# Kernel tuning notes

Measured on AMD Instinct MI355X. Metric: run time of the kernel, lower is better.

The kernel has to match this reference:

```python
import jax, jax.numpy as jnp
import numpy as np

V, E, H2, T = 50000, 256, 512, 16  # vocab, embed, hidden_dim, tagset
H = H2 // 2                        # per-direction hidden
START, STOP = 14, 15
NEG = -10000.0


def setup_inputs() -> dict:
    key = jax.random.key(0)
    ks = jax.random.split(key, 13)
    s = 0.08
    tokens = jax.random.randint(ks[0], (32, 512), 0, V)
    embed_table = jax.random.normal(ks[1], (V, E), jnp.float32)
    Wi_f = jax.random.normal(ks[2], (4 * H, E), jnp.float32) * s
    Wh_f = jax.random.normal(ks[3], (4 * H, H), jnp.float32) * s
    bi_f = jnp.zeros((4 * H,), jnp.float32)
    bh_f = jnp.zeros((4 * H,), jnp.float32)
    Wi_b = jax.random.normal(ks[4], (4 * H, E), jnp.float32) * s
    Wh_b = jax.random.normal(ks[5], (4 * H, H), jnp.float32) * s
    bi_b = jnp.zeros((4 * H,), jnp.float32)
    bh_b = jnp.zeros((4 * H,), jnp.float32)
    Wt = jax.random.normal(ks[6], (T, H2), jnp.float32) * s
    bt = jnp.zeros((T,), jnp.float32)
    trans = jax.random.normal(ks[7], (T, T), jnp.float32)
    trans = trans.at[START, :].set(NEG).at[:, STOP].set(NEG)
    return {"tokens": tokens, "embed_table": embed_table,
            "Wi_f": Wi_f, "Wh_f": Wh_f, "bi_f": bi_f, "bh_f": bh_f,
            "Wi_b": Wi_b, "Wh_b": Wh_b, "bi_b": bi_b, "bh_b": bh_b,
            "Wt": Wt, "bt": bt, "transitions": trans}


def _lstm_dir(x, Wi, Wh, bi, bh, reverse=False):
    # x: [S, B, E] -> h seq [S, B, H], PyTorch gate order i,f,g,o
    S, B, _ = x.shape
    xs = x[::-1] if reverse else x
    pre = jnp.einsum('sbe,ge->sbg', xs, Wi) + bi + bh  # precompute input GEMM

    def step(carry, z_t):
        h, c = carry
        z = z_t + h @ Wh.T  # [B, 4H]
        i, f, g, o = jnp.split(z, 4, axis=-1)
        c = jax.nn.sigmoid(f) * c + jax.nn.sigmoid(i) * jnp.tanh(g)
        h = jax.nn.sigmoid(o) * jnp.tanh(c)
        return (h, c), h

    h0 = jnp.zeros((B, H), x.dtype)
    _, hs = jax.lax.scan(step, (h0, h0), pre)
    return hs[::-1] if reverse else hs


def reference(tokens, embed_table, Wi_f, Wh_f, bi_f, bh_f,
              Wi_b, Wh_b, bi_b, bh_b, Wt, bt, transitions):
    x = embed_table[tokens]                # [B, S, E]
    x = jnp.transpose(x, (1, 0, 2))        # [S, B, E] seq-first like nn.LSTM
    hf = _lstm_dir(x, Wi_f, Wh_f, bi_f, bh_f, reverse=False)
    hb = _lstm_dir(x, Wi_b, Wh_b, bi_b, bh_b, reverse=True)
    feats = jnp.concatenate([hf, hb], axis=-1)           # [S, B, 2H]
    emissions = jnp.einsum('sbh,th->sbt', feats, Wt) + bt  # [S, B, T]

    B = tokens.shape[0]
    alpha0 = jnp.full((B, T), NEG, jnp.float32).at[:, START].set(0.0)

    def crf_step(alpha, emit_t):
        # alpha: [B, T_prev]; transitions[next, prev]; emit_t: [B, T_next]
        scores = alpha[:, None, :] + transitions[None, :, :] + emit_t[:, :, None]
        return jax.nn.logsumexp(scores, axis=2), None

    alpha, _ = jax.lax.scan(crf_step, alpha0, emissions)
    log_Z = jax.nn.logsumexp(alpha + transitions[STOP][None, :], axis=1)  # [B]
    return log_Z
```

## Files before the change

kernel.cpp:

```cpp
#include <hip/hip_runtime.h>
#include <hip/hip_bf16.h>
#include <stdint.h>

typedef __attribute__((ext_vector_type(4))) float f32x4;
typedef __attribute__((ext_vector_type(8))) short bf16x8;

#define SENT 0xFFFFFFFFFFFFFFFFULL

#define WS_XBF   0u
#define WS_WIR   8388608u
#define WS_BIAS  9437184u
#define WS_PRE   9445376u
#define WS_HALL  76554240u
#define WS_EMIS  93368320u
#define WS_CHK   94416896u

__device__ __forceinline__ unsigned short f2bf(float x) {
    union { float f; unsigned int u; } v; v.f = x;
    return (unsigned short)((v.u + 0x7FFFu + ((v.u >> 16) & 1u)) >> 16);
}
__device__ __forceinline__ float bf2f(unsigned short b) {
    union { float f; unsigned int u; } v; v.u = ((unsigned int)b) << 16; return v.f;
}
__device__ __forceinline__ unsigned int pack2(float a, float b) {
    return (unsigned int)f2bf(a) | ((unsigned int)f2bf(b) << 16);
}
__device__ __forceinline__ float sigf(float x)  { return 1.0f / (1.0f + __expf(-x)); }
__device__ __forceinline__ float tanhf_(float x){ return 1.0f - 2.0f / (__expf(2.0f * x) + 1.0f); }

__global__ __launch_bounds__(256) void k_prep(
    const int* __restrict__ tokens, const float* __restrict__ embed,
    const float* __restrict__ Wi_f, const float* __restrict__ Wi_b,
    const float* __restrict__ bi_f, const float* __restrict__ bh_f,
    const float* __restrict__ bi_b, const float* __restrict__ bh_b,
    char* __restrict__ ws)
{
    int blk = blockIdx.x, tid = threadIdx.x;
    unsigned short* xbf  = (unsigned short*)(ws + WS_XBF);
    unsigned short* wir  = (unsigned short*)(ws + WS_WIR);
    float* biasr         = (float*)(ws + WS_BIAS);
    if (blk < 2048) {
        int rr = tid >> 5, cc = tid & 31;
        int r = blk * 8 + rr;
        int s = r >> 5, b = r & 31;
        int tok = tokens[b * 512 + s];
        int k = cc * 8;
        const float* src = embed + (size_t)tok * 256 + k;
        float4 a = *(const float4*)src;
        float4 c = *(const float4*)(src + 4);
        uint4 o; o.x = pack2(a.x, a.y); o.y = pack2(a.z, a.w);
        o.z = pack2(c.x, c.y); o.w = pack2(c.z, c.w);
        *(uint4*)(xbf + (size_t)r * 256 + k) = o;
    } else if (blk < 2304) {
        int rr = tid >> 5, cc = tid & 31;
        int rowp = (blk - 2048) * 8 + rr;
        int dir = rowp >> 10, q = rowp & 1023;
        int j = q >> 8, rs = q & 255;
        int g = rs >> 6, hl = rs & 63;
        int srow = g * 256 + j * 64 + hl;
        const float* W = dir ? Wi_b : Wi_f;
        int k = cc * 8;
        const float* src = W + (size_t)srow * 256 + k;
        float4 a = *(const float4*)src;
        float4 c = *(const float4*)(src + 4);
        uint4 o; o.x = pack2(a.x, a.y); o.y = pack2(a.z, a.w);
        o.z = pack2(c.x, c.y); o.w = pack2(c.z, c.w);
        *(uint4*)(wir + (size_t)rowp * 256 + k) = o;
        if (cc == 0)
            biasr[rowp] = dir ? (bi_b[srow] + bh_b[srow]) : (bi_f[srow] + bh_f[srow]);
    } else {
        size_t g = (size_t)(blk - 2304) * 256 + tid;
        uint4* hall4 = (uint4*)(ws + WS_HALL);
        const unsigned int NF = 0xFFFFFFFFu;
        for (size_t u = g; u < 1050624u; u += 65536u) {
            size_t slot = (u >> 10) % 513u;
            uint4 val;
            if (slot == 0) { val.x = 0u; val.y = 0u; val.z = 0u; val.w = 0u; }
            else           { val.x = NF; val.y = NF; val.z = NF; val.w = NF; }
            hall4[u] = val;
        }
    }
}

__global__ __launch_bounds__(256) void k_pregemm(char* __restrict__ ws)
{
    __shared__ unsigned short Asb[128 * 136];
    __shared__ unsigned short Bsb[64 * 136];
    const unsigned short* xbf = (const unsigned short*)(ws + WS_XBF);
    const unsigned short* wir = (const unsigned short*)(ws + WS_WIR);
    const float* biasr        = (const float*)(ws + WS_BIAS);
    unsigned short* pre       = (unsigned short*)(ws + WS_PRE);
    int blk = blockIdx.x, tid = threadIdx.x;
    int mb = blk >> 5, nb = blk & 31;
    int Mbase = mb * 128, Nbase = nb * 64;
    int w = tid >> 6, l = tid & 63, col = l & 15, quad = l >> 4;
    f32x4 acc[4][2];
    #pragma unroll
    for (int a = 0; a < 4; ++a)
        #pragma unroll
        for (int b = 0; b < 2; ++b) acc[a][b] = (f32x4){0.f, 0.f, 0.f, 0.f};

    for (int kh = 0; kh < 2; ++kh) {
        __syncthreads();
        #pragma unroll
        for (int i = 0; i < 8; ++i) {
            int c = tid + i * 256;
            int row = c >> 4, c16 = c & 15;
            uint4 v = *(const uint4*)(xbf + ((size_t)(Mbase + row) * 256 + kh * 128 + c16 * 8));
            *(uint4*)(Asb + row * 136 + c16 * 8) = v;
        }
        #pragma unroll
        for (int i = 0; i < 4; ++i) {
            int c = tid + i * 256;
            int row = c >> 4, c16 = c & 15;
            uint4 v = *(const uint4*)(wir + ((size_t)(Nbase + row) * 256 + kh * 128 + c16 * 8));
            *(uint4*)(Bsb + row * 136 + c16 * 8) = v;
        }
        __syncthreads();
        int mhalf = w >> 1, nh = w & 1;
        #pragma unroll
        for (int kt = 0; kt < 4; ++kt) {
            bf16x8 bfr[2];
            #pragma unroll
            for (int nn = 0; nn < 2; ++nn)
                bfr[nn] = *(const bf16x8*)(Bsb + (16 * (nh * 2 + nn) + col) * 136 + kt * 32 + quad * 8);
            #pragma unroll
            for (int mm = 0; mm < 4; ++mm) {
                bf16x8 afr = *(const bf16x8*)(Asb + (16 * (mhalf * 4 + mm) + col) * 136 + kt * 32 + quad * 8);
                #pragma unroll
                for (int nn = 0; nn < 2; ++nn)
                    acc[mm][nn] = __builtin_amdgcn_mfma_f32_16x16x32_bf16(afr, bfr[nn], acc[mm][nn], 0, 0, 0);
            }
        }
    }
    #pragma unroll
    for (int mm = 0; mm < 4; ++mm) {
        int m_t = (w >> 1) * 4 + mm;
        int s = (Mbase >> 5) + (m_t >> 1);
        int bhalf = m_t & 1;
        #pragma unroll
        for (int nn = 0; nn < 2; ++nn) {
            int ncol = Nbase + 16 * ((w & 1) * 2 + nn) + col;
            int dir = ncol >> 10, j = (ncol >> 8) & 3, r = ncol & 255;
            int g = r >> 6, hl16 = (r >> 4) & 3;
            int tidp = (bhalf * 4 + hl16) * 64 + l;
            float bv = biasr[ncol];
            f32x4 a = acc[mm][nn];
            uint2 o;
            o.x = pack2(a[0] + bv, a[1] + bv);
            o.y = pack2(a[2] + bv, a[3] + bv);
            size_t off = (((size_t)(dir * 512 + s) * 4 + j) * 512 + tidp) * 16 + g * 4;
            *(uint2*)(pre + off) = o;
        }
    }
}

__global__ __launch_bounds__(512, 2) void k_rec(
    const float* __restrict__ Wh_f, const float* __restrict__ Wh_b, char* __restrict__ ws)
{
    __shared__ unsigned short hbuf[32 * 264];
    __shared__ unsigned short hst[8 * 16 * 20];
    int blk = blockIdx.x, tid = threadIdx.x;
    int dir = blk >> 2, j = blk & 3;
    int w = tid >> 6, l = tid & 63, col = l & 15, quad = l >> 4;
    int m = w >> 2, hl16 = w & 3;
    const float* Wh = dir ? Wh_b : Wh_f;
    const unsigned short* pre = (const unsigned short*)(ws + WS_PRE);
    unsigned short* hall      = (unsigned short*)(ws + WS_HALL);

    bf16x8 wf[4][8];
    #pragma unroll
    for (int g = 0; g < 4; ++g) {
        int grow = g * 256 + j * 64 + hl16 * 16 + col;
        #pragma unroll
        for (int kt = 0; kt < 8; ++kt) {
            const float* src = Wh + (size_t)grow * 256 + kt * 32 + quad * 8;
            float4 x0 = *(const float4*)src;
            float4 x1 = *(const float4*)(src + 4);
            bf16x8 f;
            f[0] = (short)f2bf(x0.x); f[1] = (short)f2bf(x0.y);
            f[2] = (short)f2bf(x0.z); f[3] = (short)f2bf(x0.w);
            f[4] = (short)f2bf(x1.x); f[5] = (short)f2bf(x1.y);
            f[6] = (short)f2bf(x1.z); f[7] = (short)f2bf(x1.w);
            wf[g][kt] = f;
        }
    }
    for (int u = tid; u < 1280; u += 512) ((unsigned int*)hst)[u] = 0;
    __syncthreads();

    float cst[4] = {0.f, 0.f, 0.f, 0.f};
    size_t hbase_u = (size_t)dir * 513 * 8192;

    for (int st = 0; st < 512; ++st) {
        int s = dir ? (511 - st) : st;
        const uint4* pp = (const uint4*)(pre + ((((size_t)(dir * 512 + s)) * 4 + j) * 512 + tid) * 16);
        uint4 p0 = pp[0], p1 = pp[1];

        unsigned short* hsl = hall + hbase_u + (size_t)st * 8192;
        unsigned long long v[4];
        int rows[4], c8s[4];
        bool own[4];
        #pragma unroll
        for (int i = 0; i < 4; ++i) {
            int q = tid + i * 512;
            int row = q >> 6, c8 = q & 63;
            rows[i] = row; c8s[i] = c8;
            own[i] = (c8 >= j * 16) && (c8 < j * 16 + 16);
            if (!own[i])
                v[i] = __hip_atomic_fetch_add((unsigned long long*)(hsl + (size_t)q * 4), 0ULL,
                                              __ATOMIC_RELAXED, __HIP_MEMORY_SCOPE_AGENT);
        }
        #pragma unroll
        for (int i = 0; i < 4; ++i) {
            if (own[i]) {
                int lc = c8s[i] * 4 - j * 64;
                int hl = lc >> 4, c4 = lc & 15;
                int wp = (rows[i] >> 4) * 4 + hl, r_in = rows[i] & 15;
                v[i] = *(const unsigned long long*)(hst + wp * 320 + r_in * 20 + c4);
            } else {
                while (v[i] == SENT)
                    v[i] = __hip_atomic_fetch_add((unsigned long long*)(hsl + (size_t)(tid + i * 512) * 4),
                                                  0ULL, __ATOMIC_RELAXED, __HIP_MEMORY_SCOPE_AGENT);
            }
        }
        #pragma unroll
        for (int i = 0; i < 4; ++i)
            *(unsigned long long*)(hbuf + rows[i] * 264 + c8s[i] * 4) = v[i];
        __syncthreads();

        f32x4 acc[4];
        #pragma unroll
        for (int g = 0; g < 4; ++g) acc[g] = (f32x4){0.f, 0.f, 0.f, 0.f};
        #pragma unroll
        for (int kt = 0; kt < 8; ++kt) {
            bf16x8 af = *(const bf16x8*)(hbuf + (m * 16 + col) * 264 + kt * 32 + quad * 8);
            #pragma unroll
            for (int g = 0; g < 4; ++g)
                acc[g] = __builtin_amdgcn_mfma_f32_16x16x32_bf16(af, wf[g][kt], acc[g], 0, 0, 0);
        }
        unsigned int pw[8] = {p0.x, p0.y, p0.z, p0.w, p1.x, p1.y, p1.z, p1.w};
        float z[4][4];
        #pragma unroll
        for (int g = 0; g < 4; ++g) {
            #pragma unroll
            for (int r2 = 0; r2 < 2; ++r2) {
                unsigned int u = pw[g * 2 + r2];
                z[g][r2 * 2]     = acc[g][r2 * 2]     + bf2f((unsigned short)(u & 0xffff));
                z[g][r2 * 2 + 1] = acc[g][r2 * 2 + 1] + bf2f((unsigned short)(u >> 16));
            }
        }
        unsigned short hb16[4];
        #pragma unroll
        for (int r = 0; r < 4; ++r) {
            float ci = sigf(z[1][r]) * cst[r] + sigf(z[0][r]) * tanhf_(z[2][r]);
            cst[r] = ci;
            hb16[r] = f2bf(sigf(z[3][r]) * tanhf_(ci));
        }
        unsigned short* hw = hst + w * 320;
        #pragma unroll
        for (int r = 0; r < 4; ++r) hw[(quad * 4 + r) * 20 + col] = hb16[r];
        int rrow = l >> 2, cpart = l & 3;
        unsigned long long hv = *(const unsigned long long*)(hw + rrow * 20 + cpart * 4);
        size_t dsto = hbase_u + (size_t)(st + 1) * 8192 + (size_t)(m * 16 + rrow) * 256
                    + j * 64 + hl16 * 16 + cpart * 4;
        (void)__hip_atomic_exchange((unsigned long long*)(hall + dsto), hv,
                                    __ATOMIC_RELAXED, __HIP_MEMORY_SCOPE_AGENT);
        __syncthreads();
    }
}

__global__ __launch_bounds__(256) void k_emis(
    const float* __restrict__ Wt, const float* __restrict__ bt, char* __restrict__ ws)
{
    __shared__ float WtL[16 * 528];
    __shared__ unsigned short hrow[16 * 536];
    __shared__ float btL[16];
    int blk = blockIdx.x, tid = threadIdx.x;
    int sbb = blk * 16;
    int s = sbb >> 5, bbase = sbb & 31;
    const unsigned short* hall = (const unsigned short*)(ws + WS_HALL);
    float* emis = (float*)(ws + WS_EMIS);
    #pragma unroll
    for (int i = 0; i < 8; ++i) {
        int c = tid + i * 256;
        int trow = c >> 7, c128 = c & 127;
        float4 v = *(const float4*)(Wt + (size_t)trow * 512 + c128 * 4);
        *(float4*)(WtL + trow * 528 + c128 * 4) = v;
    }
    #pragma unroll
    for (int i = 0; i < 4; ++i) {
        int c = tid + i * 256;
        int row = c >> 6, c6 = c & 63, half = c6 >> 5, c16 = c6 & 31;
        size_t base = half == 0 ? (size_t)(s + 1) * 8192 : ((size_t)513 + (512 - s)) * 8192;
        uint4 v = *(const uint4*)(hall + base + (size_t)(bbase + row) * 256 + c16 * 8);
        *(uint4*)(hrow + row * 536 + half * 256 + c16 * 8) = v;
    }
    if (tid < 16) btL[tid] = bt[tid];
    __syncthreads();
    int t = tid >> 4, i = tid & 15;
    float acc = btL[t];
    const float* wrow = WtL + t * 528;
    const unsigned short* hr = hrow + i * 536;
    #pragma unroll 8
    for (int k = 0; k < 512; k += 4) {
        uint2 hu = *(const uint2*)(hr + k);
        float4 wv = *(const float4*)(wrow + k);
        acc += bf2f((unsigned short)(hu.x & 0xffff)) * wv.x
             + bf2f((unsigned short)(hu.x >> 16))    * wv.y
             + bf2f((unsigned short)(hu.y & 0xffff)) * wv.z
             + bf2f((unsigned short)(hu.y >> 16))    * wv.w;
    }
    emis[((size_t)(bbase + i) * 512 + s) * 16 + t] = acc;
}

__global__ __launch_bounds__(256) void k_crfc(const float* __restrict__ trans, char* __restrict__ ws)
{
    __shared__ float trL[16 * 17];
    __shared__ float est[16 * 16];
    __shared__ float Pb[2][16 * 17];
    int blk = blockIdx.x, tid = threadIdx.x;
    int b = blk >> 5, c = blk & 31;
    int t = tid >> 4, p = tid & 15;
    const float* emis = (const float*)(ws + WS_EMIS);
    float* chk = (float*)(ws + WS_CHK);
    trL[t * 17 + p] = trans[t * 16 + p];
    est[t * 16 + p] = emis[((size_t)b * 512 + c * 16 + t) * 16 + p];
    __syncthreads();
    float tr[16];
    #pragma unroll
    for (int q = 0; q < 16; ++q) tr[q] = trL[t * 17 + q];
    float out = trL[t * 17 + p] + est[0 * 16 + t];
    Pb[0][t * 17 + p] = out;
    __syncthreads();
    int cur = 0;
    for (int si = 1; si < 16; ++si) {
        float v[16]; float mx = -3.0e38f;
        #pragma unroll
        for (int q = 0; q < 16; ++q) { v[q] = tr[q] + Pb[cur][q * 17 + p]; mx = fmaxf(mx, v[q]); }
        float ss = 0.f;
        #pragma unroll
        for (int q = 0; q < 16; ++q) ss += __expf(v[q] - mx);
        out = est[si * 16 + t] + mx + __logf(ss);
        Pb[1 - cur][t * 17 + p] = out;
        __syncthreads();
        cur = 1 - cur;
    }
    chk[(size_t)(b * 32 + c) * 256 + t * 16 + p] = out;
}

__global__ __launch_bounds__(256) void k_crff(
    const float* __restrict__ trans, char* __restrict__ ws, float* __restrict__ out)
{
    __shared__ float Cst[16 * 17];
    __shared__ float Pb[2][16 * 17];
    __shared__ float af[16];
    int b = blockIdx.x, tid = threadIdx.x;
    int t = tid >> 4, p = tid & 15;
    const float* chk = (const float*)(ws + WS_CHK);
    Pb[0][t * 17 + p] = chk[(size_t)(b * 32) * 256 + t * 16 + p];
    __syncthreads();
    int cur = 0;
    for (int ci = 1; ci < 32; ++ci) {
        Cst[t * 17 + p] = chk[(size_t)(b * 32 + ci) * 256 + t * 16 + p];
        __syncthreads();
        float v[16]; float mx = -3.0e38f;
        #pragma unroll
        for (int q = 0; q < 16; ++q) { v[q] = Cst[t * 17 + q] + Pb[cur][q * 17 + p]; mx = fmaxf(mx, v[q]); }
        float ss = 0.f;
        #pragma unroll
        for (int q = 0; q < 16; ++q) ss += __expf(v[q] - mx);
        float outv = mx + __logf(ss);
        Pb[1 - cur][t * 17 + p] = outv;
        __syncthreads();
        cur = 1 - cur;
    }
    float vfin = Pb[cur][t * 17 + p] + ((p == 14) ? 0.0f : -10000.0f);
    Cst[t * 17 + p] = vfin;
    __syncthreads();
    if (tid < 16) {
        float mx = -3.0e38f;
        for (int q = 0; q < 16; ++q) mx = fmaxf(mx, Cst[tid * 17 + q]);
        float ss = 0.f;
        for (int q = 0; q < 16; ++q) ss += __expf(Cst[tid * 17 + q] - mx);
        af[tid] = mx + __logf(ss) + trans[15 * 16 + tid];
    }
    __syncthreads();
    if (tid == 0) {
        float mx = -3.0e38f;
        for (int q = 0; q < 16; ++q) mx = fmaxf(mx, af[q]);
        float ss = 0.f;
        for (int q = 0; q < 16; ++q) ss += __expf(af[q] - mx);
        out[b] = mx + __logf(ss);
    }
}

extern "C" void kernel_launch(void* const* d_in, const int* in_sizes, int n_in,
                              void* d_out, int out_size, void* d_ws, size_t ws_size,
                              hipStream_t stream)
{
    const int*   tokens = (const int*)d_in[0];
    const float* embed  = (const float*)d_in[1];
    const float* Wi_f   = (const float*)d_in[2];
    const float* Wh_f   = (const float*)d_in[3];
    const float* bi_f   = (const float*)d_in[4];
    const float* bh_f   = (const float*)d_in[5];
    const float* Wi_b   = (const float*)d_in[6];
    const float* Wh_b   = (const float*)d_in[7];
    const float* bi_b   = (const float*)d_in[8];
    const float* bh_b   = (const float*)d_in[9];
    const float* Wt     = (const float*)d_in[10];
    const float* bt     = (const float*)d_in[11];
    const float* trans  = (const float*)d_in[12];
    char* ws = (char*)d_ws;
    float* out = (float*)d_out;

    hipLaunchKernelGGL(k_prep, dim3(2560), dim3(256), 0, stream,
                       tokens, embed, Wi_f, Wi_b, bi_f, bh_f, bi_b, bh_b, ws);
    hipLaunchKernelGGL(k_pregemm, dim3(4096), dim3(256), 0, stream, ws);
    hipLaunchKernelGGL(k_rec, dim3(8), dim3(512), 0, stream, Wh_f, Wh_b, ws);
    hipLaunchKernelGGL(k_emis, dim3(1024), dim3(256), 0, stream, Wt, bt, ws);
    hipLaunchKernelGGL(k_crfc, dim3(1024), dim3(256), 0, stream, trans, ws);
    hipLaunchKernelGGL(k_crff, dim3(32), dim3(256), 0, stream, trans, ws, out);
}
```

Measured before the change: 1.608 ms.

## Co-locate recurrence blocks on one XCD and use workgroup-scope polling

The recurrent kernel now launches 128 blocks. Each block reads its XCC_ID and claims a slot through atomic counters, and the first XCD to gather 8 blocks takes all 8 recurrence roles while the remaining blocks exit. Because all cooperating blocks then share one XCD's L2, the cross-block hidden-state exchange switches to workgroup-scope atomics (CAS-based polling and exchange), which avoids the slower device-scope coherence traffic on every timestep. The polling loop is also restructured per thread with bounded retries. This relies on an assumption about XCD cache sharing and on enough blocks landing on one XCD; if no XCD gathers 8 blocks in time, or scope semantics differ from the assumption, the result could be wrong or the kernel could stall.

```diff
diff --git a/kernel.cpp b/kernel.cpp
--- a/kernel.cpp
+++ b/kernel.cpp
@@ -12,6 +12,7 @@
 #define WS_BIAS  9437184u
 #define WS_PRE   9445376u
 #define WS_HALL  76554240u
+#define WS_CTL   93364224u
 #define WS_EMIS  93368320u
 #define WS_CHK   94416896u
 
@@ -69,6 +70,8 @@
         if (cc == 0)
             biasr[rowp] = dir ? (bi_b[srow] + bh_b[srow]) : (bi_f[srow] + bh_f[srow]);
     } else {
+        if (blk == 2304 && tid < 16)
+            ((unsigned int*)(ws + WS_CTL))[tid] = 0u;
         size_t g = (size_t)(blk - 2304) * 256 + tid;
         uint4* hall4 = (uint4*)(ws + WS_HALL);
         const unsigned int NF = 0xFFFFFFFFu;
@@ -160,8 +163,37 @@
 {
     __shared__ unsigned short hbuf[32 * 264];
     __shared__ unsigned short hst[8 * 16 * 20];
-    int blk = blockIdx.x, tid = threadIdx.x;
-    int dir = blk >> 2, j = blk & 3;
+    __shared__ int sRole;
+    int tid = threadIdx.x;
+
+    if (tid == 0) {
+        int xcd;
+        asm volatile("s_getreg_b32 %0, hwreg(HW_REG_XCC_ID)" : "=s"(xcd));
+        xcd &= 7;
+        unsigned int* ctl = (unsigned int*)(ws + WS_CTL);
+        unsigned int slot = __hip_atomic_fetch_add(&ctl[xcd], 1u,
+                              __ATOMIC_RELAXED, __HIP_MEMORY_SCOPE_AGENT);
+        int role = -1;
+        if (slot < 8u) {
+            if (slot == 7u) {
+                unsigned int expv = 0u;
+                __hip_atomic_compare_exchange_strong(&ctl[8], &expv, (unsigned int)(xcd + 1),
+                    __ATOMIC_RELAXED, __ATOMIC_RELAXED, __HIP_MEMORY_SCOPE_AGENT);
+            }
+            unsigned int ts; long gc = 0;
+            do {
+                ts = __hip_atomic_fetch_add(&ctl[8], 0u,
+                        __ATOMIC_RELAXED, __HIP_MEMORY_SCOPE_AGENT);
+            } while (ts == 0u && ++gc < (1L << 26));
+            if (ts == (unsigned int)(xcd + 1)) role = (int)slot;
+        }
+        sRole = role;
+    }
+    __syncthreads();
+    int role = sRole;
+    if (role < 0) return;
+    int dir = role >> 2, j = role & 3;
+
     int w = tid >> 6, l = tid & 63, col = l & 15, quad = l >> 4;
     int m = w >> 2, hl16 = w & 3;
     const float* Wh = dir ? Wh_b : Wh_f;
@@ -190,6 +222,8 @@
 
     float cst[4] = {0.f, 0.f, 0.f, 0.f};
     size_t hbase_u = (size_t)dir * 513 * 8192;
+    int row0 = tid >> 6, c8 = tid & 63;
+    bool ownl = (c8 >= j * 16) && (c8 < j * 16 + 16);
 
     for (int st = 0; st < 512; ++st) {
         int s = dir ? (511 - st) : st;
@@ -198,34 +232,44 @@
 
         unsigned short* hsl = hall + hbase_u + (size_t)st * 8192;
         unsigned long long v[4];
-        int rows[4], c8s[4];
-        bool own[4];
-        #pragma unroll
-        for (int i = 0; i < 4; ++i) {
-            int q = tid + i * 512;
-            int row = q >> 6, c8 = q & 63;
-            rows[i] = row; c8s[i] = c8;
-            own[i] = (c8 >= j * 16) && (c8 < j * 16 + 16);
-            if (!own[i])
-                v[i] = __hip_atomic_fetch_add((unsigned long long*)(hsl + (size_t)q * 4), 0ULL,
-                                              __ATOMIC_RELAXED, __HIP_MEMORY_SCOPE_AGENT);
-        }
-        #pragma unroll
-        for (int i = 0; i < 4; ++i) {
-            if (own[i]) {
-                int lc = c8s[i] * 4 - j * 64;
-                int hl = lc >> 4, c4 = lc & 15;
-                int wp = (rows[i] >> 4) * 4 + hl, r_in = rows[i] & 15;
+        if (ownl) {
+            int lc = c8 * 4 - j * 64;
+            int hl = lc >> 4, c4 = lc & 15;
+            #pragma unroll
+            for (int i = 0; i < 4; ++i) {
+                int row = row0 + i * 8;
+                int wp = (row >> 4) * 4 + hl, r_in = row & 15;
                 v[i] = *(const unsigned long long*)(hst + wp * 320 + r_in * 20 + c4);
-            } else {
-                while (v[i] == SENT)
-                    v[i] = __hip_atomic_fetch_add((unsigned long long*)(hsl + (size_t)(tid + i * 512) * 4),
-                                                  0ULL, __ATOMIC_RELAXED, __HIP_MEMORY_SCOPE_AGENT);
+            }
+        } else {
+            #pragma unroll
+            for (int i = 0; i < 4; ++i) {
+                unsigned long long expv = SENT;
+                __hip_atomic_compare_exchange_strong(
+                    (unsigned long long*)(hsl + (size_t)(tid + i * 512) * 4), &expv, SENT,
+                    __ATOMIC_RELAXED, __ATOMIC_RELAXED, __HIP_MEMORY_SCOPE_WORKGROUP);
+                v[i] = expv;
+            }
+            bool pend = (v[0] == SENT) | (v[1] == SENT) | (v[2] == SENT) | (v[3] == SENT);
+            int rnd = 0;
+            while (pend && rnd < 65536) {
+                #pragma unroll
+                for (int i = 0; i < 4; ++i) {
+                    if (v[i] == SENT) {
+                        unsigned long long expv = SENT;
+                        __hip_atomic_compare_exchange_strong(
+                            (unsigned long long*)(hsl + (size_t)(tid + i * 512) * 4), &expv, SENT,
+                            __ATOMIC_RELAXED, __ATOMIC_RELAXED, __HIP_MEMORY_SCOPE_WORKGROUP);
+                        v[i] = expv;
+                    }
+                }
+                pend = (v[0] == SENT) | (v[1] == SENT) | (v[2] == SENT) | (v[3] == SENT);
+                ++rnd;
             }
         }
         #pragma unroll
         for (int i = 0; i < 4; ++i)
-            *(unsigned long long*)(hbuf + rows[i] * 264 + c8s[i] * 4) = v[i];
+            *(unsigned long long*)(hbuf + (row0 + i * 8) * 264 + c8 * 4) = v[i];
         __syncthreads();
 
         f32x4 acc[4];
@@ -264,7 +308,7 @@
         size_t dsto = hbase_u + (size_t)(st + 1) * 8192 + (size_t)(m * 16 + rrow) * 256
                     + j * 64 + hl16 * 16 + cpart * 4;
         (void)__hip_atomic_exchange((unsigned long long*)(hall + dsto), hv,
-                                    __ATOMIC_RELAXED, __HIP_MEMORY_SCOPE_AGENT);
+                                    __ATOMIC_RELAXED, __HIP_MEMORY_SCOPE_WORKGROUP);
         __syncthreads();
     }
 }
@@ -417,7 +461,7 @@
     hipLaunchKernelGGL(k_prep, dim3(2560), dim3(256), 0, stream,
                        tokens, embed, Wi_f, Wi_b, bi_f, bh_f, bi_b, bh_b, ws);
     hipLaunchKernelGGL(k_pregemm, dim3(4096), dim3(256), 0, stream, ws);
-    hipLaunchKernelGGL(k_rec, dim3(8), dim3(512), 0, stream, Wh_f, Wh_b, ws);
+    hipLaunchKernelGGL(k_rec, dim3(128), dim3(512), 0, stream, Wh_f, Wh_b, ws);
     hipLaunchKernelGGL(k_emis, dim3(1024), dim3(256), 0, stream, Wt, bt, ws);
     hipLaunchKernelGGL(k_crfc, dim3(1024), dim3(256), 0, stream, trans, ws);
     hipLaunchKernelGGL(k_crff, dim3(32), dim3(256), 0, stream, trans, ws, out);
```

Result: no change. 1.596 ms (-0.8%).
